# Optimization experiments

Hardware: AMD Instinct MI355X
Metric: run time of the kernel (lower is better)

## Reference

```python
import jax, jax.numpy as jnp
from jax import lax
import numpy as np

T_STEPS, C_IN, H_IN, W_IN = 15, 6, 256, 256
C_OUT, KSIZE = 64, 5
THRESH = 15.0   # conv_t[0]
KWTA = 5        # ks[0]
INH_R = 3       # inh_radiuses[0]


def setup_inputs() -> dict:
    key = jax.random.key(0)
    k1, k2 = jax.random.split(key)
    # cumulative binary spike-wave: once a unit spikes it stays on (SpykeTorch convention)
    bern = jax.random.uniform(k1, (T_STEPS, C_IN, H_IN, W_IN)) < 0.05
    spikes = (jnp.cumsum(bern.astype(jnp.int32), axis=0) > 0).astype(jnp.float32)
    # SpykeTorch Convolution init: N(0.8, 0.05)
    w1 = 0.8 + 0.05 * jax.random.normal(k2, (C_OUT, C_IN, KSIZE, KSIZE), dtype=jnp.float32)
    return {"input": spikes, "w1": w1, "current_layer_id": 1}


def pointwise_inhibition(thr_pot):
    # thr_pot: (T, C, H, W). Keep, at each spatial position, only the feature
    # with the earliest spike (ties broken by max potential); zero the rest.
    T = thr_pot.shape[0]
    C = thr_pot.shape[1]
    max_vals = jnp.max(thr_pot, axis=1, keepdims=True)            # (T,1,H,W)
    max_idx = jnp.argmax(thr_pot, axis=1, keepdims=True)          # (T,1,H,W)
    clamp_pot = jnp.sign(max_vals)                                # (T,1,H,W) in {0,1}
    earliest = jnp.clip((T - clamp_pot.sum(axis=0, keepdims=True)).astype(jnp.int32), 0, T - 1)  # (1,1,H,W)
    winners = jnp.take_along_axis(max_idx, earliest, axis=0)      # (1,1,H,W)
    onehot = (jnp.arange(C)[None, :, None, None] == winners[:, 0])  # (1,C,H,W)
    coef = onehot.astype(thr_pot.dtype) * clamp_pot[-1:]          # zero where no spike at last step
    return thr_pot * coef


def get_k_winners(pot, spk, kwta, inh_radius):
    # pot, spk: (T, C, H, W). Returns (kwta, 3) int winners (c, h, w); -1 rows = no winner.
    T, C, H, W = pot.shape
    earliest = jnp.clip((T - spk.sum(axis=0, keepdims=True)).astype(jnp.int32), 0, T - 1)
    values = jnp.take_along_axis(pot, earliest, axis=0)           # (1,C,H,W)
    trunc = spk * values
    v = trunc.max() * T
    trunc = trunc + spk * v
    total = trunc.sum(axis=0)                                     # (C,H,W)
    rows = jnp.arange(H)
    cols = jnp.arange(W)

    def step(total, _):
        idx = jnp.argmax(total)
        val = total.reshape(-1)[idx]
        c = idx // (H * W)
        rem = idx % (H * W)
        h = rem // W
        w = rem % W
        winner = jnp.where(val != 0,
                           jnp.stack([c, h, w]),
                           jnp.full((3,), -1, dtype=idx.dtype))
        total = total.at[c].set(0.0)
        box = (((rows >= h - inh_radius) & (rows <= h + inh_radius))[:, None]
               & ((cols >= w - inh_radius) & (cols <= w + inh_radius))[None, :])
        total = jnp.where(box[None, :, :], 0.0, total)            # columnar spatial inhibition
        return total, winner

    _, winners = lax.scan(step, total, None, length=kwta)
    return winners


def reference(input, w1, current_layer_id):
    # training path, current_layer_id == 1
    x = jnp.pad(input.astype(jnp.float32), ((0, 0), (0, 0), (2, 2), (2, 2)))  # sf.pad (2,2,2,2)
    pot = lax.conv_general_dilated(x, w1, (1, 1), 'VALID',
                                   dimension_numbers=('NCHW', 'OIHW', 'NCHW'))  # (T,64,256,256)
    pot = jnp.where(pot < THRESH, 0.0, pot)   # sf.fire -> thresholded potentials
    pot = pointwise_inhibition(pot)
    spk = jnp.sign(pot)
    winners = get_k_winners(pot, spk, KWTA, INH_R)
    return spk, pot, winners
```

## Files before the change

kernel.cpp:

```cpp
#include <hip/hip_runtime.h>
#include <hip/hip_cooperative_groups.h>
#include <stdint.h>

namespace cg = cooperative_groups;

static constexpr int T_STEPS = 15;
static constexpr int C_IN = 6;
static constexpr int C_OUT = 64;
static constexpr int H = 256;
static constexpr int W = 256;
static constexpr int NPOS = H * W;
static constexpr int NTAP = 150;
#define DTHRESH 15.0

typedef float vfloat4 __attribute__((ext_vector_type(4)));

static constexpr size_t WS_FT     = 0;
static constexpr size_t WS_SERIES = 393216;
static constexpr size_t WS_WINC   = WS_SERIES + (size_t)NPOS*16*4;
static constexpr size_t WS_NMAP   = WS_WINC + (size_t)NPOS;
static constexpr size_t WS_VAL    = WS_NMAP + (size_t)NPOS;
static constexpr size_t WS_RED    = WS_VAL + (size_t)NPOS*8;
static constexpr size_t WS_RIX    = WS_RED + 768*8;
static constexpr size_t WS_NEED   = WS_RIX + 512*4;

__global__ __launch_bounds__(256) void ft_kernel(const float* __restrict__ x,
                                                 uint8_t* __restrict__ ft) {
    int i = blockIdx.x * 256 + threadIdx.x;
    if (i >= C_IN * NPOS) return;
    int f = 15;
    #pragma unroll
    for (int t = T_STEPS - 1; t >= 0; --t) {
        if (x[(size_t)t * (C_IN * NPOS) + i] > 0.0f) f = t;
    }
    ft[i] = (uint8_t)f;
}

__global__ __launch_bounds__(256, 4) void conv_kernel(
        const float* __restrict__ w1, const uint8_t* __restrict__ ftg,
        float* __restrict__ series_ws, int8_t* __restrict__ winc_ws,
        uint8_t* __restrict__ nmap_ws, double* __restrict__ val_ws)
{
    __shared__ float w_lds[NTAP * 64];
    __shared__ uint8_t ft_lds[6 * 5 * 20];
    __shared__ alignas(16) unsigned cnt_lds[4][16];
    __shared__ alignas(16) unsigned short sorted_lds[4][200];

    int tid = threadIdx.x;
    int bid = blockIdx.x;
    int h  = bid >> 4;
    int w0 = (bid & 15) << 4;

    for (int i = tid; i < C_OUT * NTAP; i += 256) {
        int o = i / NTAP;
        int tap = i - o * NTAP;
        w_lds[tap * 64 + o] = w1[i];
    }
    for (int i = tid; i < 600; i += 256) {
        int c = i / 100;
        int r = i - c * 100;
        int kh = r / 20;
        int j  = r - kh * 20;
        int gh = h - 2 + kh;
        int gw = w0 - 2 + j;
        uint8_t v = 15;
        if (gh >= 0 && gh < H && gw >= 0 && gw < W) v = ftg[c * NPOS + gh * W + gw];
        ft_lds[(c * 5 + kh) * 20 + j] = v;
    }
    __syncthreads();

    int lane = tid & 63;
    int wvi  = tid >> 6;
    unsigned* cnt = cnt_lds[wvi];
    unsigned short* srt = sorted_lds[wvi];

    for (int iter = 0; iter < 4; ++iter) {
        int xl = iter * 4 + wvi;
        int p  = h * W + w0 + xl;

        if (lane < 16) cnt[lane] = 0;

        int tap0 = lane, tap1 = lane + 64, tap2 = lane + 128;
        auto ftv = [&](int tap) -> unsigned {
            int c = tap / 25;
            int r = tap - c * 25;
            int kh = r / 5;
            int kw = r - kh * 5;
            return ft_lds[(c * 5 + kh) * 20 + xl + kw];
        };
        unsigned f0 = ftv(tap0);
        unsigned f1 = ftv(tap1);
        unsigned f2 = (tap2 < NTAP) ? ftv(tap2) : 15u;
        unsigned r0 = 0, r1 = 0, r2 = 0;
        if (f0 < 15u) r0 = atomicAdd(&cnt[f0], 1u);
        if (f1 < 15u) r1 = atomicAdd(&cnt[f1], 1u);
        if (f2 < 15u) r2 = atomicAdd(&cnt[f2], 1u);

        uint4 c4[4];
        #pragma unroll
        for (int i = 0; i < 4; ++i) c4[i] = ((const uint4*)cnt)[i];
        unsigned cv_t[16];
        #pragma unroll
        for (int i = 0; i < 4; ++i) {
            cv_t[4*i+0] = c4[i].x; cv_t[4*i+1] = c4[i].y;
            cv_t[4*i+2] = c4[i].z; cv_t[4*i+3] = c4[i].w;
        }
        int kt[15];
        #pragma unroll
        for (int t = 0; t < 15; ++t) kt[t] = (int)__builtin_amdgcn_readfirstlane(cv_t[t]);

        unsigned st0 = 0, st1 = 0, st2 = 0;
        #pragma unroll
        for (int t = 0; t < 15; ++t) {
            unsigned a = (cv_t[t] + 3u) & ~3u;
            if ((unsigned)t < f0) st0 += a;
            if ((unsigned)t < f1) st1 += a;
            if ((unsigned)t < f2) st2 += a;
        }
        if (f0 < 15u) srt[st0 + r0] = (unsigned short)(tap0 << 6);
        if (f1 < 15u) srt[st1 + r1] = (unsigned short)(tap1 << 6);
        if (f2 < 15u) srt[st2 + r2] = (unsigned short)(tap2 << 6);

        double run = 0.0, cvv = 0.0;
        int tc = 127;
        float ser[15];
        int A = 0;
        #pragma unroll
        for (int t = 0; t < 15; ++t) {
            int k = kt[t];
            for (int q = 0; q < k; q += 4) {
                uint2 pr = *(const uint2*)(srt + A + q);
                unsigned e0 = pr.x & 0xFFFFu, e1 = pr.x >> 16;
                unsigned e2 = pr.y & 0xFFFFu, e3 = pr.y >> 16;
                e0 = min(e0, 9536u); e1 = min(e1, 9536u);
                e2 = min(e2, 9536u); e3 = min(e3, 9536u);
                float wa = w_lds[e0 + lane];
                float wb = w_lds[e1 + lane];
                float wcf = w_lds[e2 + lane];
                float wd = w_lds[e3 + lane];
                double p0 = (double)wa;
                double p1 = (q + 1 < k) ? (double)wb : 0.0;
                double p2 = (q + 2 < k) ? (double)wcf : 0.0;
                double p3 = (q + 3 < k) ? (double)wd : 0.0;
                run += ((p0 + p1) + (p2 + p3));
            }
            A += (k + 3) & ~3;
            ser[t] = (float)run;
            bool cross_now = (tc == 127) && (run >= DTHRESH);
            if (cross_now) { tc = t; cvv = run; }
        }

        int e = tc;
        #pragma unroll
        for (int off = 32; off >= 1; off >>= 1) e = min(e, __shfl_xor(e, off));
        int wc = -1;
        double val = 0.0;
        if (e < 15) {
            double vl = (tc == e) ? cvv : 0.0;
            double m = vl;
            #pragma unroll
            for (int off = 32; off >= 1; off >>= 1) m = fmax(m, __shfl_xor(m, off));
            unsigned long long mk = __ballot(vl == m);
            wc = __ffsll(mk) - 1;
            val = m;

            float ov = 0.0f;
            #pragma unroll
            for (int t = 0; t < 15; ++t) {
                float sv = __shfl(ser[t], wc);
                if (lane == t) ov = sv;
            }
            if (lane < e) ov = 0.0f;
            if (lane < 15) series_ws[p * 16 + lane] = ov;
        }
        if (lane == 0) {
            winc_ws[p] = (int8_t)wc;
            nmap_ws[p] = (uint8_t)(wc >= 0 ? (15 - e) : 0);
            if (wc >= 0) val_ws[p] = val;
        }
    }
}

__global__ __launch_bounds__(256) void kwin_kernel(
        const int8_t* __restrict__ winc, const uint8_t* __restrict__ nmap,
        const double* __restrict__ val, float* __restrict__ outw,
        double* __restrict__ redv, unsigned* __restrict__ redi)
{
    cg::grid_group grid = cg::this_grid();
    const int tid  = threadIdx.x;
    const int bid  = blockIdx.x;
    const int p    = (bid << 8) | tid;
    const int lane = tid & 63, wvi = tid >> 6;

    __shared__ double   s_v[4];
    __shared__ unsigned s_i[4];

    const int    c     = winc[p];
    const bool   owner = (c >= 0);
    const double vp    = owner ? val[p] : 0.0;
    const double nm    = (double)nmap[p];
    const int    hh    = p >> 8;
    const int    ww    = p & 255;
    bool alive = owner;

    double mv = vp;
    #pragma unroll
    for (int off = 32; off >= 1; off >>= 1) mv = fmax(mv, __shfl_xor(mv, off));
    if (lane == 0) s_v[wvi] = mv;
    __syncthreads();
    if (tid == 0)
        redv[512 + bid] = fmax(fmax(s_v[0], s_v[1]), fmax(s_v[2], s_v[3]));
    grid.sync();
    double pv = redv[512 + tid];
    #pragma unroll
    for (int off = 32; off >= 1; off >>= 1) pv = fmax(pv, __shfl_xor(pv, off));
    if (lane == 0) s_v[wvi] = pv;
    __syncthreads();
    const double v = 15.0 * fmax(fmax(s_v[0], s_v[1]), fmax(s_v[2], s_v[3]));

    for (int r = 0; r < 5; ++r) {
        __syncthreads();
        const int par = r & 1;

        double   bv = -1.0;
        unsigned bi = 0xFFFFFFFFu;
        if (alive) {
            bv = nm * (vp + v);
            bi = ((unsigned)c << 16) | (unsigned)p;
        }
        #pragma unroll
        for (int off = 32; off >= 1; off >>= 1) {
            double   ov = __shfl_xor(bv, off);
            unsigned oi = __shfl_xor(bi, off);
            if (ov > bv || (ov == bv && oi < bi)) { bv = ov; bi = oi; }
        }
        if (lane == 0) { s_v[wvi] = bv; s_i[wvi] = bi; }
        __syncthreads();
        if (tid == 0) {
            double bbv = s_v[0]; unsigned bbi = s_i[0];
            #pragma unroll
            for (int i = 1; i < 4; ++i)
                if (s_v[i] > bbv || (s_v[i] == bbv && s_i[i] < bbi)) { bbv = s_v[i]; bbi = s_i[i]; }
            redv[par * 256 + bid] = bbv;
            redi[par * 256 + bid] = bbi;
        }
        grid.sync();

        double   gv = redv[par * 256 + tid];
        unsigned gi = redi[par * 256 + tid];
        #pragma unroll
        for (int off = 32; off >= 1; off >>= 1) {
            double   ov = __shfl_xor(gv, off);
            unsigned oi = __shfl_xor(gi, off);
            if (ov > gv || (ov == gv && oi < gi)) { gv = ov; gi = oi; }
        }
        if (lane == 0) { s_v[wvi] = gv; s_i[wvi] = gi; }
        __syncthreads();
        double bbv = s_v[0]; unsigned bbi = s_i[0];
        #pragma unroll
        for (int i = 1; i < 4; ++i)
            if (s_v[i] > bbv || (s_v[i] == bbv && s_i[i] < bbi)) { bbv = s_v[i]; bbi = s_i[i]; }

        const bool valid = (bbv > 0.0);
        if (bid == 0 && tid == 0) {
            int wc2 = (int)(bbi >> 16), pp = (int)(bbi & 0xFFFFu);
            outw[r * 3 + 0] = valid ? (float)wc2       : -1.0f;
            outw[r * 3 + 1] = valid ? (float)(pp >> 8) : -1.0f;
            outw[r * 3 + 2] = valid ? (float)(pp & 255): -1.0f;
        }
        if (valid) {
            const int wc2 = (int)(bbi >> 16);
            const int wp  = (int)(bbi & 0xFFFFu);
            const int wh  = wp >> 8, wwv = wp & 255;
            if (c == wc2 || (hh >= wh - 3 && hh <= wh + 3 &&
                             ww >= wwv - 3 && ww <= wwv + 3)) alive = false;
        }
    }
}

__global__ __launch_bounds__(256) void expand_kernel(
        const int8_t* __restrict__ winc, const float* __restrict__ series,
        float* __restrict__ spk, float* __restrict__ pot)
{
    int idx4 = blockIdx.x * 256 + threadIdx.x;
    int w4 = idx4 & 63;
    int h  = (idx4 >> 6) & 255;
    int c  = (idx4 >> 14) & 63;
    int t  = idx4 >> 20;
    int pbase = h * W + (w4 << 2);
    uint32_t wcs = *reinterpret_cast<const uint32_t*>(winc + pbase);
    vfloat4 pv = (vfloat4)(0.0f);
    vfloat4 sv = (vfloat4)(0.0f);
    #pragma unroll
    for (int e2 = 0; e2 < 4; ++e2) {
        int8_t wcb = (int8_t)((wcs >> (8 * e2)) & 0xFFu);
        if ((int)wcb == c) {
            float xv = series[(size_t)(pbase + e2) * 16 + t];
            pv[e2] = xv;
            sv[e2] = (xv > 0.f) ? 1.0f : 0.0f;
        }
    }
    reinterpret_cast<vfloat4*>(spk)[idx4] = sv;
    reinterpret_cast<vfloat4*>(pot)[idx4] = pv;
}

extern "C" void kernel_launch(void* const* d_in, const int* in_sizes, int n_in,
                              void* d_out, int out_size, void* d_ws, size_t ws_size,
                              hipStream_t stream)
{
    if (ws_size < WS_NEED) return;

    const float* x  = (const float*)d_in[0];
    const float* w1 = (const float*)d_in[1];
    uint8_t* ws = (uint8_t*)d_ws;
    uint8_t* ftg    = ws + WS_FT;
    float*   series = (float*)(ws + WS_SERIES);
    int8_t*  winc   = (int8_t*)(ws + WS_WINC);
    uint8_t* nmap   = (uint8_t*)(ws + WS_NMAP);
    double*  val    = (double*)(ws + WS_VAL);
    double*  redv   = (double*)(ws + WS_RED);
    unsigned* redi  = (unsigned*)(ws + WS_RIX);

    float* spk  = (float*)d_out;
    float* pot  = spk + (size_t)T_STEPS * C_OUT * NPOS;
    float* outw = pot + (size_t)T_STEPS * C_OUT * NPOS;

    hipLaunchKernelGGL(ft_kernel,     dim3(1536),  dim3(256),  0, stream, x, ftg);
    hipLaunchKernelGGL(conv_kernel,   dim3(4096),  dim3(256),  0, stream, w1, ftg, series, winc, nmap, val);

    void* kargs[] = { (void*)&winc, (void*)&nmap, (void*)&val,
                      (void*)&outw, (void*)&redv, (void*)&redi };
    hipLaunchCooperativeKernel((const void*)kwin_kernel, dim3(256), dim3(256), kargs, 0, stream);

    hipLaunchKernelGGL(expand_kernel, dim3(61440), dim3(256),  0, stream, winc, series, spk, pot);
}
```

Measured before the change: 867.8 us.

## Shrink kWTA cooperative grid and use byte tap indices with zero-padded weights

The kWTA kernel now runs on 64 blocks with four positions per thread. It drops the initial grid-wide max reduction and its grid.sync by ranking on a key of nmap*2048+val, which is meant to preserve the original nm*(vp+v) ordering. The cross-block reduction is done by a single wave. In the conv kernel, sorted tap lists are stored as bytes, and padding slots point at an added zero weight row, which removes the per-element min clamps and the conditional masking in the inner accumulation loop. The new key is only order-equivalent if potentials stay below 2048, and the padding writes add a few LDS stores per position.

After: 760.0 us. 1.14x faster.

```diff
diff --git a/kernel.cpp b/kernel.cpp
--- a/kernel.cpp
+++ b/kernel.cpp
@@ -21,8 +21,8 @@
 static constexpr size_t WS_NMAP   = WS_WINC + (size_t)NPOS;
 static constexpr size_t WS_VAL    = WS_NMAP + (size_t)NPOS;
 static constexpr size_t WS_RED    = WS_VAL + (size_t)NPOS*8;
-static constexpr size_t WS_RIX    = WS_RED + 768*8;
-static constexpr size_t WS_NEED   = WS_RIX + 512*4;
+static constexpr size_t WS_RIX    = WS_RED + 128*8;
+static constexpr size_t WS_NEED   = WS_RIX + 128*4;
 
 __global__ __launch_bounds__(256) void ft_kernel(const float* __restrict__ x,
                                                  uint8_t* __restrict__ ft) {
@@ -41,10 +41,10 @@
         float* __restrict__ series_ws, int8_t* __restrict__ winc_ws,
         uint8_t* __restrict__ nmap_ws, double* __restrict__ val_ws)
 {
-    __shared__ float w_lds[NTAP * 64];
+    __shared__ float w_lds[(NTAP + 1) * 64];
     __shared__ uint8_t ft_lds[6 * 5 * 20];
     __shared__ alignas(16) unsigned cnt_lds[4][16];
-    __shared__ alignas(16) unsigned short sorted_lds[4][200];
+    __shared__ alignas(8) uint8_t sorted_lds[4][200];
 
     int tid = threadIdx.x;
     int bid = blockIdx.x;
@@ -56,6 +56,7 @@
         int tap = i - o * NTAP;
         w_lds[tap * 64 + o] = w1[i];
     }
+    if (tid < 64) w_lds[NTAP * 64 + tid] = 0.0f;
     for (int i = tid; i < 600; i += 256) {
         int c = i / 100;
         int r = i - c * 100;
@@ -72,7 +73,7 @@
     int lane = tid & 63;
     int wvi  = tid >> 6;
     unsigned* cnt = cnt_lds[wvi];
-    unsigned short* srt = sorted_lds[wvi];
+    uint8_t* srt = sorted_lds[wvi];
 
     for (int iter = 0; iter < 4; ++iter) {
         int xl = iter * 4 + wvi;
@@ -109,17 +110,26 @@
         #pragma unroll
         for (int t = 0; t < 15; ++t) kt[t] = (int)__builtin_amdgcn_readfirstlane(cv_t[t]);
 
-        unsigned st0 = 0, st1 = 0, st2 = 0;
+        unsigned st0 = 0, st1 = 0, st2 = 0, stp = 0;
         #pragma unroll
         for (int t = 0; t < 15; ++t) {
             unsigned a = (cv_t[t] + 3u) & ~3u;
             if ((unsigned)t < f0) st0 += a;
             if ((unsigned)t < f1) st1 += a;
             if ((unsigned)t < f2) st2 += a;
-        }
-        if (f0 < 15u) srt[st0 + r0] = (unsigned short)(tap0 << 6);
-        if (f1 < 15u) srt[st1 + r1] = (unsigned short)(tap1 << 6);
-        if (f2 < 15u) srt[st2 + r2] = (unsigned short)(tap2 << 6);
+            if (t < lane) stp += a;
+        }
+        if (f0 < 15u) srt[st0 + r0] = (uint8_t)tap0;
+        if (f1 < 15u) srt[st1 + r1] = (uint8_t)tap1;
+        if (f2 < 15u) srt[st2 + r2] = (uint8_t)tap2;
+
+        if (lane < 15) {
+            unsigned kk = cnt[lane];
+            unsigned a4 = (kk + 3u) & ~3u;
+            if (kk     < a4) srt[stp + kk]     = (uint8_t)NTAP;
+            if (kk + 1 < a4) srt[stp + kk + 1] = (uint8_t)NTAP;
+            if (kk + 2 < a4) srt[stp + kk + 2] = (uint8_t)NTAP;
+        }
 
         double run = 0.0, cvv = 0.0;
         int tc = 127;
@@ -129,20 +139,12 @@
         for (int t = 0; t < 15; ++t) {
             int k = kt[t];
             for (int q = 0; q < k; q += 4) {
-                uint2 pr = *(const uint2*)(srt + A + q);
-                unsigned e0 = pr.x & 0xFFFFu, e1 = pr.x >> 16;
-                unsigned e2 = pr.y & 0xFFFFu, e3 = pr.y >> 16;
-                e0 = min(e0, 9536u); e1 = min(e1, 9536u);
-                e2 = min(e2, 9536u); e3 = min(e3, 9536u);
-                float wa = w_lds[e0 + lane];
-                float wb = w_lds[e1 + lane];
-                float wcf = w_lds[e2 + lane];
-                float wd = w_lds[e3 + lane];
-                double p0 = (double)wa;
-                double p1 = (q + 1 < k) ? (double)wb : 0.0;
-                double p2 = (q + 2 < k) ? (double)wcf : 0.0;
-                double p3 = (q + 3 < k) ? (double)wd : 0.0;
-                run += ((p0 + p1) + (p2 + p3));
+                unsigned pr = *(const unsigned*)(srt + A + q);
+                float wa  = w_lds[((pr       & 0xFFu) << 6) + lane];
+                float wb  = w_lds[(((pr >> 8) & 0xFFu) << 6) + lane];
+                float wcf = w_lds[(((pr >> 16) & 0xFFu) << 6) + lane];
+                float wd  = w_lds[(( pr >> 24        ) << 6) + lane];
+                run += (((double)wa + (double)wb) + ((double)wcf + (double)wd));
             }
             A += (k + 3) & ~3;
             ser[t] = (float)run;
@@ -189,34 +191,28 @@
     cg::grid_group grid = cg::this_grid();
     const int tid  = threadIdx.x;
     const int bid  = blockIdx.x;
-    const int p    = (bid << 8) | tid;
     const int lane = tid & 63, wvi = tid >> 6;
 
     __shared__ double   s_v[4];
     __shared__ unsigned s_i[4];
 
-    const int    c     = winc[p];
-    const bool   owner = (c >= 0);
-    const double vp    = owner ? val[p] : 0.0;
-    const double nm    = (double)nmap[p];
-    const int    hh    = p >> 8;
-    const int    ww    = p & 255;
-    bool alive = owner;
-
-    double mv = vp;
+    int     pc[4];
+    int     phh[4], pww[4];
+    double  key[4];
+    unsigned idx[4];
+    bool    alive[4];
     #pragma unroll
-    for (int off = 32; off >= 1; off >>= 1) mv = fmax(mv, __shfl_xor(mv, off));
-    if (lane == 0) s_v[wvi] = mv;
-    __syncthreads();
-    if (tid == 0)
-        redv[512 + bid] = fmax(fmax(s_v[0], s_v[1]), fmax(s_v[2], s_v[3]));
-    grid.sync();
-    double pv = redv[512 + tid];
-    #pragma unroll
-    for (int off = 32; off >= 1; off >>= 1) pv = fmax(pv, __shfl_xor(pv, off));
-    if (lane == 0) s_v[wvi] = pv;
-    __syncthreads();
-    const double v = 15.0 * fmax(fmax(s_v[0], s_v[1]), fmax(s_v[2], s_v[3]));
+    for (int k = 0; k < 4; ++k) {
+        const int p = (k << 14) | (bid << 8) | tid;
+        const int c = winc[p];
+        alive[k] = (c >= 0);
+        const double vp = alive[k] ? val[p] : 0.0;
+        key[k]  = (double)nmap[p] * 2048.0 + vp;
+        idx[k]  = ((unsigned)c << 16) | (unsigned)p;
+        pc[k]   = c;
+        phh[k]  = p >> 8;
+        pww[k]  = p & 255;
+    }
 
     for (int r = 0; r < 5; ++r) {
         __syncthreads();
@@ -224,9 +220,11 @@
 
         double   bv = -1.0;
         unsigned bi = 0xFFFFFFFFu;
-        if (alive) {
-            bv = nm * (vp + v);
-            bi = ((unsigned)c << 16) | (unsigned)p;
+        #pragma unroll
+        for (int k = 0; k < 4; ++k) {
+            if (alive[k] && (key[k] > bv || (key[k] == bv && idx[k] < bi))) {
+                bv = key[k]; bi = idx[k];
+            }
         }
         #pragma unroll
         for (int off = 32; off >= 1; off >>= 1) {
@@ -241,25 +239,25 @@
             #pragma unroll
             for (int i = 1; i < 4; ++i)
                 if (s_v[i] > bbv || (s_v[i] == bbv && s_i[i] < bbi)) { bbv = s_v[i]; bbi = s_i[i]; }
-            redv[par * 256 + bid] = bbv;
-            redi[par * 256 + bid] = bbi;
+            redv[par * 64 + bid] = bbv;
+            redi[par * 64 + bid] = bbi;
         }
         grid.sync();
 
-        double   gv = redv[par * 256 + tid];
-        unsigned gi = redi[par * 256 + tid];
-        #pragma unroll
-        for (int off = 32; off >= 1; off >>= 1) {
-            double   ov = __shfl_xor(gv, off);
-            unsigned oi = __shfl_xor(gi, off);
-            if (ov > gv || (ov == gv && oi < gi)) { gv = ov; gi = oi; }
-        }
-        if (lane == 0) { s_v[wvi] = gv; s_i[wvi] = gi; }
+        if (wvi == 0) {
+            double   gv = redv[par * 64 + lane];
+            unsigned gi = redi[par * 64 + lane];
+            #pragma unroll
+            for (int off = 32; off >= 1; off >>= 1) {
+                double   ov = __shfl_xor(gv, off);
+                unsigned oi = __shfl_xor(gi, off);
+                if (ov > gv || (ov == gv && oi < gi)) { gv = ov; gi = oi; }
+            }
+            if (lane == 0) { s_v[0] = gv; s_i[0] = gi; }
+        }
         __syncthreads();
-        double bbv = s_v[0]; unsigned bbi = s_i[0];
-        #pragma unroll
-        for (int i = 1; i < 4; ++i)
-            if (s_v[i] > bbv || (s_v[i] == bbv && s_i[i] < bbi)) { bbv = s_v[i]; bbi = s_i[i]; }
+        const double   bbv = s_v[0];
+        const unsigned bbi = s_i[0];
 
         const bool valid = (bbv > 0.0);
         if (bid == 0 && tid == 0) {
@@ -272,8 +270,11 @@
             const int wc2 = (int)(bbi >> 16);
             const int wp  = (int)(bbi & 0xFFFFu);
             const int wh  = wp >> 8, wwv = wp & 255;
-            if (c == wc2 || (hh >= wh - 3 && hh <= wh + 3 &&
-                             ww >= wwv - 3 && ww <= wwv + 3)) alive = false;
+            #pragma unroll
+            for (int k = 0; k < 4; ++k) {
+                if (pc[k] == wc2 || (phh[k] >= wh - 3 && phh[k] <= wh + 3 &&
+                                     pww[k] >= wwv - 3 && pww[k] <= wwv + 3)) alive[k] = false;
+            }
         }
     }
 }
@@ -330,7 +331,7 @@
 
     void* kargs[] = { (void*)&winc, (void*)&nmap, (void*)&val,
                       (void*)&outw, (void*)&redv, (void*)&redi };
-    hipLaunchCooperativeKernel((const void*)kwin_kernel, dim3(256), dim3(256), kargs, 0, stream);
+    hipLaunchCooperativeKernel((const void*)kwin_kernel, dim3(64), dim3(256), kargs, 0, stream);
 
     hipLaunchKernelGGL(expand_kernel, dim3(61440), dim3(256),  0, stream, winc, series, spk, pot);
 }
```
